# Kernel optimization log

Hardware: AMD Instinct MI355X
Metric: run time of the kernel (lower is better)

## Reference

```python
import jax, jax.numpy as jnp
import numpy as np
from jax import lax

B, S, H, I, E, TOP_K = 4, 4096, 2048, 1024, 8, 2


def setup_inputs() -> dict:
    key = jax.random.key(0)
    k1, k2, k3, k4, k5 = jax.random.split(key, 5)
    scale = 0.02  # realistic init scale so router logits are well-conditioned
    return {
        "x": jax.random.normal(k1, (B, S, H), dtype=jnp.float32),
        "gate_w": jax.random.normal(k2, (E, H), dtype=jnp.float32) * scale,
        "wg": jax.random.normal(k3, (E, H, I), dtype=jnp.float32) * scale,
        "wu": jax.random.normal(k4, (E, H, I), dtype=jnp.float32) * scale,
        "wd": jax.random.normal(k5, (E, I, H), dtype=jnp.float32) * scale,
    }


def reference(x, gate_w, wg, wu, wd):
    b, s, h = x.shape
    xt = x.reshape(b * s, h)                      # [T, H]
    router_logits = xt @ gate_w.T                 # [T, E]
    probs = jax.nn.softmax(router_logits, axis=-1)
    topk_w, topk_idx = lax.top_k(probs, TOP_K)    # [T, K]
    T = xt.shape[0]
    # combine[t, e] = routing weight of expert e for token t (0 if not in top-k)
    combine = jnp.zeros((T, E), xt.dtype).at[
        jnp.arange(T)[:, None], topk_idx
    ].set(topk_w)

    # scan over experts; each step is one grouped SwiGLU MLP over all tokens,
    # weighted by the (mostly-zero) combine column -> identical math to the
    # torch gather/index_add dispatch.
    def step(acc, ew):
        wgi, wui, wdi, c = ew                     # [H,I],[H,I],[I,H],[T]
        hdn = jax.nn.silu(xt @ wgi) * (xt @ wui)  # [T, I]
        return acc + c[:, None] * (hdn @ wdi), None

    acc, _ = lax.scan(step, jnp.zeros_like(xt), (wg, wu, wd, combine.T))
    return acc.reshape(b, s, h), router_logits
```

## Files before the change

### kernel.cpp

```cpp
#include <hip/hip_runtime.h>

#define T_TOK 16384
#define H_DIM 2048
#define I_DIM 1024
#define E_NUM 8

static const size_t F_WGT = 0;
static const size_t F_WUT = 33554432ull;
static const size_t F_XH  = 67108864ull;
static const size_t F_Y2  = 0;
static const size_t F_WDT = 134217728ull;
static const size_t F_HDN = 167772160ull;
static const size_t F_TOK = 234881024ull;
static const size_t F_WT  = 235405312ull;
static const size_t F_IDX = 235929600ull;
static const size_t F_CNT = 236060672ull;

typedef float f32x4 __attribute__((ext_vector_type(4)));
typedef _Float16 f16x8 __attribute__((ext_vector_type(8)));
typedef _Float16 f16x4 __attribute__((ext_vector_type(4)));

__device__ __forceinline__ void gload_lds16(const void* g, void* l) {
  __builtin_amdgcn_global_load_lds(
      (const __attribute__((address_space(1))) unsigned int*)g,
      (__attribute__((address_space(3))) unsigned int*)l, 16, 0, 0);
}

__global__ __launch_bounds__(256) void wconv_kernel(
    const float* __restrict__ wg, const float* __restrict__ wu,
    const float* __restrict__ wd, _Float16* __restrict__ wgT,
    _Float16* __restrict__ wuT, _Float16* __restrict__ wdT) {
  const int bx = blockIdx.x;
  const int w = bx >> 12;
  const int r2 = bx & 4095;
  const int e = r2 >> 9;
  const int t = r2 & 511;

  const float* src;
  _Float16* dst;
  int R, C;
  if (w == 0)      { src = wg; dst = wgT; R = H_DIM; C = I_DIM; }
  else if (w == 1) { src = wu; dst = wuT; R = H_DIM; C = I_DIM; }
  else             { src = wd; dst = wdT; R = I_DIM; C = H_DIM; }
  src += (size_t)e * R * C;
  dst += (size_t)e * R * C;

  const int tiles_c = C >> 6;
  const int tr = t / tiles_c;
  const int tc = t % tiles_c;

  __shared__ float tile[64][65];
  const int tid = threadIdx.x;

#pragma unroll
  for (int c = 0; c < 4; ++c) {
    const int q = c * 256 + tid;
    const int row = q >> 4;
    const int col4 = (q & 15) * 4;
    const float4 v = *(const float4*)(src + (size_t)(tr * 64 + row) * C + tc * 64 + col4);
    tile[row][col4 + 0] = v.x;
    tile[row][col4 + 1] = v.y;
    tile[row][col4 + 2] = v.z;
    tile[row][col4 + 3] = v.w;
  }
  __syncthreads();
#pragma unroll
  for (int c = 0; c < 4; ++c) {
    const int q = c * 256 + tid;
    const int row = q >> 4;
    const int col4 = (q & 15) * 4;
    f16x4 o = { (_Float16)tile[col4 + 0][row], (_Float16)tile[col4 + 1][row],
                (_Float16)tile[col4 + 2][row], (_Float16)tile[col4 + 3][row] };
    *(f16x4*)(dst + (size_t)(tc * 64 + row) * R + tr * 64 + col4) = o;
  }
}

__global__ __launch_bounds__(256) void router_kernel(
    const float* __restrict__ x, const float* __restrict__ gw,
    float* __restrict__ logits, int* __restrict__ tok_list,
    float* __restrict__ wt_list, int* __restrict__ idx2,
    int* __restrict__ counts, _Float16* __restrict__ xh) {
  const int lane = threadIdx.x & 63;
  const int wave = threadIdx.x >> 6;
  const int t = blockIdx.x * 4 + wave;
  const float* xr = x + (size_t)t * H_DIM;

  float xv[32];
#pragma unroll
  for (int j = 0; j < 32; ++j) xv[j] = xr[lane + j * 64];

  _Float16* xhr = xh + (size_t)t * H_DIM;
#pragma unroll
  for (int j = 0; j < 32; ++j) xhr[lane + j * 64] = (_Float16)xv[j];

  float lg[E_NUM];
#pragma unroll
  for (int e = 0; e < E_NUM; ++e) {
    const float* gr = gw + e * H_DIM;
    float s = 0.f;
#pragma unroll
    for (int j = 0; j < 32; ++j) s += xv[j] * gr[lane + j * 64];
#pragma unroll
    for (int off = 32; off > 0; off >>= 1) s += __shfl_xor(s, off, 64);
    lg[e] = s;
  }

  if (lane == 0) {
#pragma unroll
    for (int e = 0; e < E_NUM; ++e) logits[(size_t)t * E_NUM + e] = lg[e];
    float mx = lg[0];
#pragma unroll
    for (int e = 1; e < E_NUM; ++e) mx = fmaxf(mx, lg[e]);
    float se = 0.f;
#pragma unroll
    for (int e = 0; e < E_NUM; ++e) se += expf(lg[e] - mx);
    int i1 = 0; float b1 = lg[0];
#pragma unroll
    for (int e = 1; e < E_NUM; ++e) { if (lg[e] > b1) { b1 = lg[e]; i1 = e; } }
    int i2 = -1; float b2 = -1e30f;
#pragma unroll
    for (int e = 0; e < E_NUM; ++e) { if (e != i1 && lg[e] > b2) { b2 = lg[e]; i2 = e; } }
    const float p1 = expf(b1 - mx) / se;
    const float p2 = expf(b2 - mx) / se;
    int pos = atomicAdd(&counts[i1], 1);
    tok_list[i1 * T_TOK + pos] = t;
    wt_list[i1 * T_TOK + pos] = p1;
    idx2[t * 2] = (i1 << 16) | pos;
    pos = atomicAdd(&counts[i2], 1);
    tok_list[i2 * T_TOK + pos] = t;
    wt_list[i2 * T_TOK + pos] = p2;
    idx2[t * 2 + 1] = (i2 << 16) | pos;
  }
}

__global__ __launch_bounds__(256) void gemm1_kernel(
    const _Float16* __restrict__ xh, const _Float16* __restrict__ wgT,
    const _Float16* __restrict__ wuT, const int* __restrict__ tok_list,
    const int* __restrict__ counts, _Float16* __restrict__ hdn) {
  const int bx = blockIdx.x;
  const int cb = bx & 7;
  const int rb = (bx >> 3) & 127;
  const int e = bx >> 10;
  const int n_e = counts[e];
  const int row0 = rb * 128;
  if (row0 >= n_e) return;
  int goff = 0;
#pragma unroll
  for (int j = 0; j < E_NUM; ++j) goff += (j < e) ? counts[j] : 0;
  const int rem = min(128, n_e - row0);

  __shared__ int toks[128];
  __shared__ __attribute__((aligned(16))) _Float16 As[128 * 64];
  __shared__ __attribute__((aligned(16))) _Float16 Bg[128 * 64];
  __shared__ __attribute__((aligned(16))) _Float16 Bu[128 * 64];

  const int tid = threadIdx.x;
  if (tid < 128) {
    int idx = row0 + tid;
    if (idx > n_e - 1) idx = n_e - 1;
    toks[tid] = tok_list[e * T_TOK + idx];
  }
  __syncthreads();

  const int lane = tid & 63;
  const int wid = tid >> 6;
  const int wr = (wid >> 1) * 64;
  const int wcl = (wid & 1) * 64;
  const int n0 = cb * 128;

  const _Float16* wgTe = wgT + ((size_t)e * I_DIM + n0) * H_DIM;
  const _Float16* wuTe = wuT + ((size_t)e * I_DIM + n0) * H_DIM;

  const _Float16* aptr[4];
  int boff[4];
  int dofs[4];
#pragma unroll
  for (int c = 0; c < 4; ++c) {
    const int q = c * 256 + tid;
    const int rr = q >> 3;
    const int ch = q & 7;
    const int sch = ch ^ (rr & 7);
    aptr[c] = xh + (size_t)toks[rr] * H_DIM + sch * 8;
    boff[c] = rr * H_DIM + sch * 8;
    dofs[c] = q * 8;
  }

  const f32x4 z4 = {0.f, 0.f, 0.f, 0.f};
  f32x4 accg[4][4], accu[4][4];
#pragma unroll
  for (int m = 0; m < 4; ++m)
#pragma unroll
    for (int n = 0; n < 4; ++n) { accg[m][n] = z4; accu[m][n] = z4; }

  const int cl = lane & 15;
  const int kq = lane >> 4;

  for (int k0 = 0; k0 < H_DIM; k0 += 64) {
#pragma unroll
    for (int c = 0; c < 4; ++c) gload_lds16(aptr[c] + k0, As + dofs[c]);
#pragma unroll
    for (int c = 0; c < 4; ++c) gload_lds16(wgTe + boff[c] + k0, Bg + dofs[c]);
#pragma unroll
    for (int c = 0; c < 4; ++c) gload_lds16(wuTe + boff[c] + k0, Bu + dofs[c]);
    __syncthreads();

#pragma unroll
    for (int ks = 0; ks < 2; ++ks) {
      f16x8 af[4], bg[4], bu[4];
#pragma unroll
      for (int m = 0; m < 4; ++m) {
        const int row = wr + m * 16 + cl;
        af[m] = *(const f16x8*)(As + row * 64 + (((ks * 4 + kq) ^ (cl & 7)) * 8));
      }
#pragma unroll
      for (int n = 0; n < 4; ++n) {
        const int row = wcl + n * 16 + cl;
        const int off = row * 64 + (((ks * 4 + kq) ^ (cl & 7)) * 8);
        bg[n] = *(const f16x8*)(Bg + off);
        bu[n] = *(const f16x8*)(Bu + off);
      }
#pragma unroll
      for (int m = 0; m < 4; ++m)
#pragma unroll
        for (int n = 0; n < 4; ++n) {
          accg[m][n] = __builtin_amdgcn_mfma_f32_16x16x32_f16(af[m], bg[n], accg[m][n], 0, 0, 0);
          accu[m][n] = __builtin_amdgcn_mfma_f32_16x16x32_f16(af[m], bu[n], accu[m][n], 0, 0, 0);
        }
    }
    __syncthreads();
  }

  const int rq = lane >> 4;
#pragma unroll
  for (int m = 0; m < 4; ++m) {
#pragma unroll
    for (int r = 0; r < 4; ++r) {
      const int row = wr + m * 16 + rq * 4 + r;
      if (row < rem) {
        const size_t grow = (size_t)(goff + row0 + row);
#pragma unroll
        for (int n = 0; n < 4; ++n) {
          const float g = accg[m][n][r];
          const float u = accu[m][n][r];
          const float h = g / (1.f + __expf(-g)) * u;
          hdn[grow * I_DIM + n0 + wcl + n * 16 + cl] = (_Float16)h;
        }
      }
    }
  }
}

__global__ __launch_bounds__(256) void gemm2_kernel(
    const _Float16* __restrict__ hdn, const _Float16* __restrict__ wdT,
    const int* __restrict__ tok_list, const float* __restrict__ wt_list,
    const int* __restrict__ counts, _Float16* __restrict__ y2) {
  const int bx = blockIdx.x;
  const int nb = bx & 15;
  const int rb = (bx >> 4) & 127;
  const int e = bx >> 11;
  const int n_e = counts[e];
  const int row0 = rb * 128;
  if (row0 >= n_e) return;
  int goff = 0;
#pragma unroll
  for (int j = 0; j < E_NUM; ++j) goff += (j < e) ? counts[j] : 0;
  const int rem = min(128, n_e - row0);

  __shared__ float wts[128];
  __shared__ __attribute__((aligned(16))) _Float16 As[128 * 64];
  __shared__ __attribute__((aligned(16))) _Float16 Bs[128 * 64];

  const int tid = threadIdx.x;
  if (tid < 128) {
    int idx = row0 + tid;
    const bool valid = (idx < n_e);
    wts[tid] = valid ? wt_list[e * T_TOK + min(idx, n_e - 1)] : 0.f;
  }
  __syncthreads();

  const int lane = tid & 63;
  const int wid = tid >> 6;
  const int wr = (wid >> 1) * 64;
  const int wcl = (wid & 1) * 64;
  const int h0 = nb * 128;

  const _Float16* wdTe = wdT + ((size_t)e * H_DIM + h0) * I_DIM;
  const _Float16* hdnb = hdn + (size_t)(goff + row0) * I_DIM;

  const _Float16* aptr[4];
  int boff[4];
  int dofs[4];
#pragma unroll
  for (int c = 0; c < 4; ++c) {
    const int q = c * 256 + tid;
    const int rr = q >> 3;
    const int ch = q & 7;
    const int sch = ch ^ (rr & 7);
    const int rrc = min(rr, rem - 1);
    aptr[c] = hdnb + (size_t)rrc * I_DIM + sch * 8;
    boff[c] = rr * I_DIM + sch * 8;
    dofs[c] = q * 8;
  }

  const f32x4 z4 = {0.f, 0.f, 0.f, 0.f};
  f32x4 acc[4][4];
#pragma unroll
  for (int m = 0; m < 4; ++m)
#pragma unroll
    for (int n = 0; n < 4; ++n) acc[m][n] = z4;

  const int cl = lane & 15;
  const int kq = lane >> 4;

  for (int k0 = 0; k0 < I_DIM; k0 += 64) {
#pragma unroll
    for (int c = 0; c < 4; ++c) gload_lds16(aptr[c] + k0, As + dofs[c]);
#pragma unroll
    for (int c = 0; c < 4; ++c) gload_lds16(wdTe + boff[c] + k0, Bs + dofs[c]);
    __syncthreads();

#pragma unroll
    for (int ks = 0; ks < 2; ++ks) {
      f16x8 af[4], bf[4];
#pragma unroll
      for (int m = 0; m < 4; ++m) {
        const int row = wr + m * 16 + cl;
        af[m] = *(const f16x8*)(As + row * 64 + (((ks * 4 + kq) ^ (cl & 7)) * 8));
      }
#pragma unroll
      for (int n = 0; n < 4; ++n) {
        const int row = wcl + n * 16 + cl;
        bf[n] = *(const f16x8*)(Bs + row * 64 + (((ks * 4 + kq) ^ (cl & 7)) * 8));
      }
#pragma unroll
      for (int m = 0; m < 4; ++m)
#pragma unroll
        for (int n = 0; n < 4; ++n)
          acc[m][n] = __builtin_amdgcn_mfma_f32_16x16x32_f16(af[m], bf[n], acc[m][n], 0, 0, 0);
    }
    __syncthreads();
  }

  const int rq = lane >> 4;
#pragma unroll
  for (int m = 0; m < 4; ++m) {
#pragma unroll
    for (int r = 0; r < 4; ++r) {
      const int row = wr + m * 16 + rq * 4 + r;
      if (row < rem) {
        const float w = wts[row];
        _Float16* yrow = y2 + (size_t)(goff + row0 + row) * H_DIM + h0 + wcl;
#pragma unroll
        for (int n = 0; n < 4; ++n)
          yrow[n * 16 + cl] = (_Float16)(acc[m][n][r] * w);
      }
    }
  }
}

__global__ __launch_bounds__(256) void combine_kernel(
    const _Float16* __restrict__ y2, const int* __restrict__ idx2,
    const int* __restrict__ counts, float* __restrict__ out) {
  const int t = blockIdx.x;
  int pref[E_NUM];
  int run = 0;
#pragma unroll
  for (int e = 0; e < E_NUM; ++e) { pref[e] = run; run += counts[e]; }
  const int p0 = idx2[t * 2];
  const int p1 = idx2[t * 2 + 1];
  const size_t r0 = (size_t)(pref[p0 >> 16] + (p0 & 0xFFFF)) * H_DIM;
  const size_t r1 = (size_t)(pref[p1 >> 16] + (p1 & 0xFFFF)) * H_DIM;
  const int o = threadIdx.x * 8;
  const f16x8 a = *(const f16x8*)(y2 + r0 + o);
  const f16x8 b = *(const f16x8*)(y2 + r1 + o);
  float* orow = out + (size_t)t * H_DIM + o;
  float4 lo = { (float)a[0] + (float)b[0], (float)a[1] + (float)b[1],
                (float)a[2] + (float)b[2], (float)a[3] + (float)b[3] };
  float4 hi = { (float)a[4] + (float)b[4], (float)a[5] + (float)b[5],
                (float)a[6] + (float)b[6], (float)a[7] + (float)b[7] };
  *(float4*)orow = lo;
  *(float4*)(orow + 4) = hi;
}

extern "C" void kernel_launch(void* const* d_in, const int* in_sizes, int n_in,
                              void* d_out, int out_size, void* d_ws, size_t ws_size,
                              hipStream_t stream) {
  (void)in_sizes; (void)n_in; (void)out_size; (void)ws_size;
  const float* x      = (const float*)d_in[0];
  const float* gate_w = (const float*)d_in[1];
  const float* wg     = (const float*)d_in[2];
  const float* wu     = (const float*)d_in[3];
  const float* wd     = (const float*)d_in[4];
  float* out0 = (float*)d_out;
  float* out1 = out0 + (size_t)T_TOK * H_DIM;

  char* ws = (char*)d_ws;
  _Float16* wgT = (_Float16*)(ws + F_WGT);
  _Float16* wuT = (_Float16*)(ws + F_WUT);
  _Float16* xh  = (_Float16*)(ws + F_XH);
  _Float16* y2  = (_Float16*)(ws + F_Y2);
  _Float16* wdT = (_Float16*)(ws + F_WDT);
  _Float16* hdn = (_Float16*)(ws + F_HDN);
  int* tok_list = (int*)(ws + F_TOK);
  float* wt_list = (float*)(ws + F_WT);
  int* idx2 = (int*)(ws + F_IDX);
  int* counts = (int*)(ws + F_CNT);

  hipMemsetAsync(counts, 0, 64, stream);
  wconv_kernel<<<12288, 256, 0, stream>>>(wg, wu, wd, wgT, wuT, wdT);
  router_kernel<<<T_TOK / 4, 256, 0, stream>>>(x, gate_w, out1, tok_list, wt_list, idx2, counts, xh);
  gemm1_kernel<<<E_NUM * 128 * 8, 256, 0, stream>>>(xh, wgT, wuT, tok_list, counts, hdn);
  gemm2_kernel<<<E_NUM * 128 * 16, 256, 0, stream>>>(hdn, wdT, tok_list, wt_list, counts, y2);
  combine_kernel<<<T_TOK, 256, 0, stream>>>(y2, idx2, counts, out0);
}
```

Measured before the change: 1.630 ms.

## Double-buffer LDS tiles with K=32 steps to overlap loads with MFMA

```diff
diff --git a/kernel.cpp b/kernel.cpp
--- a/kernel.cpp
+++ b/kernel.cpp
@@ -150,9 +150,9 @@
   const int rem = min(128, n_e - row0);
 
   __shared__ int toks[128];
-  __shared__ __attribute__((aligned(16))) _Float16 As[128 * 64];
-  __shared__ __attribute__((aligned(16))) _Float16 Bg[128 * 64];
-  __shared__ __attribute__((aligned(16))) _Float16 Bu[128 * 64];
+  __shared__ __attribute__((aligned(16))) _Float16 As[2][128 * 32];
+  __shared__ __attribute__((aligned(16))) _Float16 Bg[2][128 * 32];
+  __shared__ __attribute__((aligned(16))) _Float16 Bu[2][128 * 32];
 
   const int tid = threadIdx.x;
   if (tid < 128) {
@@ -171,17 +171,16 @@
   const _Float16* wgTe = wgT + ((size_t)e * I_DIM + n0) * H_DIM;
   const _Float16* wuTe = wuT + ((size_t)e * I_DIM + n0) * H_DIM;
 
-  const _Float16* aptr[4];
-  int boff[4];
-  int dofs[4];
-#pragma unroll
-  for (int c = 0; c < 4; ++c) {
+  const _Float16* asrc[2];
+  int bofs[2], dofs[2];
+#pragma unroll
+  for (int c = 0; c < 2; ++c) {
     const int q = c * 256 + tid;
-    const int rr = q >> 3;
-    const int ch = q & 7;
-    const int sch = ch ^ (rr & 7);
-    aptr[c] = xh + (size_t)toks[rr] * H_DIM + sch * 8;
-    boff[c] = rr * H_DIM + sch * 8;
+    const int rr = q >> 2;
+    const int ch = q & 3;
+    const int sch = ch ^ ((rr >> 1) & 3);
+    asrc[c] = xh + (size_t)toks[rr] * H_DIM + sch * 8;
+    bofs[c] = rr * H_DIM + sch * 8;
     dofs[c] = q * 8;
   }
 
@@ -195,39 +194,61 @@
   const int cl = lane & 15;
   const int kq = lane >> 4;
 
-  for (int k0 = 0; k0 < H_DIM; k0 += 64) {
-#pragma unroll
-    for (int c = 0; c < 4; ++c) gload_lds16(aptr[c] + k0, As + dofs[c]);
-#pragma unroll
-    for (int c = 0; c < 4; ++c) gload_lds16(wgTe + boff[c] + k0, Bg + dofs[c]);
-#pragma unroll
-    for (int c = 0; c < 4; ++c) gload_lds16(wuTe + boff[c] + k0, Bu + dofs[c]);
-    __syncthreads();
-
-#pragma unroll
-    for (int ks = 0; ks < 2; ++ks) {
-      f16x8 af[4], bg[4], bu[4];
-#pragma unroll
-      for (int m = 0; m < 4; ++m) {
-        const int row = wr + m * 16 + cl;
-        af[m] = *(const f16x8*)(As + row * 64 + (((ks * 4 + kq) ^ (cl & 7)) * 8));
+  int aoff[4], boffr[4];
+#pragma unroll
+  for (int m = 0; m < 4; ++m) {
+    const int row = wr + m * 16 + cl;
+    aoff[m] = row * 32 + ((kq ^ ((row >> 1) & 3)) * 8);
+  }
+#pragma unroll
+  for (int n = 0; n < 4; ++n) {
+    const int row = wcl + n * 16 + cl;
+    boffr[n] = row * 32 + ((kq ^ ((row >> 1) & 3)) * 8);
+  }
+
+#pragma unroll
+  for (int c = 0; c < 2; ++c) {
+    gload_lds16(asrc[c], &As[0][0] + dofs[c]);
+    gload_lds16(wgTe + bofs[c], &Bg[0][0] + dofs[c]);
+    gload_lds16(wuTe + bofs[c], &Bu[0][0] + dofs[c]);
+  }
+  asm volatile("s_waitcnt vmcnt(0)" ::: "memory");
+  __builtin_amdgcn_s_barrier();
+  __builtin_amdgcn_sched_barrier(0);
+
+  const int NK = H_DIM / 32;
+  for (int t = 0; t < NK; ++t) {
+    const int cur = t & 1;
+    if (t + 1 < NK) {
+      const int kn = (t + 1) * 32;
+#pragma unroll
+      for (int c = 0; c < 2; ++c) {
+        gload_lds16(asrc[c] + kn, &As[cur ^ 1][0] + dofs[c]);
+        gload_lds16(wgTe + bofs[c] + kn, &Bg[cur ^ 1][0] + dofs[c]);
+        gload_lds16(wuTe + bofs[c] + kn, &Bu[cur ^ 1][0] + dofs[c]);
       }
+    }
+    const _Float16* Ac = &As[cur][0];
+    const _Float16* Gc = &Bg[cur][0];
+    const _Float16* Uc = &Bu[cur][0];
+    f16x8 af[4], bg[4], bu[4];
+#pragma unroll
+    for (int m = 0; m < 4; ++m) af[m] = *(const f16x8*)(Ac + aoff[m]);
+#pragma unroll
+    for (int n = 0; n < 4; ++n) {
+      bg[n] = *(const f16x8*)(Gc + boffr[n]);
+      bu[n] = *(const f16x8*)(Uc + boffr[n]);
+    }
+#pragma unroll
+    for (int m = 0; m < 4; ++m)
 #pragma unroll
       for (int n = 0; n < 4; ++n) {
-        const int row = wcl + n * 16 + cl;
-        const int off = row * 64 + (((ks * 4 + kq) ^ (cl & 7)) * 8);
-        bg[n] = *(const f16x8*)(Bg + off);
-        bu[n] = *(const f16x8*)(Bu + off);
+        accg[m][n] = __builtin_amdgcn_mfma_f32_16x16x32_f16(af[m], bg[n], accg[m][n], 0, 0, 0);
+        accu[m][n] = __builtin_amdgcn_mfma_f32_16x16x32_f16(af[m], bu[n], accu[m][n], 0, 0, 0);
       }
-#pragma unroll
-      for (int m = 0; m < 4; ++m)
-#pragma unroll
-        for (int n = 0; n < 4; ++n) {
-          accg[m][n] = __builtin_amdgcn_mfma_f32_16x16x32_f16(af[m], bg[n], accg[m][n], 0, 0, 0);
-          accu[m][n] = __builtin_amdgcn_mfma_f32_16x16x32_f16(af[m], bu[n], accu[m][n], 0, 0, 0);
-        }
-    }
-    __syncthreads();
+    asm volatile("s_waitcnt vmcnt(0)" ::: "memory");
+    __builtin_amdgcn_s_barrier();
+    __builtin_amdgcn_sched_barrier(0);
   }
 
   const int rq = lane >> 4;
@@ -267,8 +288,8 @@
   const int rem = min(128, n_e - row0);
 
   __shared__ float wts[128];
-  __shared__ __attribute__((aligned(16))) _Float16 As[128 * 64];
-  __shared__ __attribute__((aligned(16))) _Float16 Bs[128 * 64];
+  __shared__ __attribute__((aligned(16))) _Float16 As[2][128 * 32];
+  __shared__ __attribute__((aligned(16))) _Float16 Bs[2][128 * 32];
 
   const int tid = threadIdx.x;
   if (tid < 128) {
@@ -287,18 +308,17 @@
   const _Float16* wdTe = wdT + ((size_t)e * H_DIM + h0) * I_DIM;
   const _Float16* hdnb = hdn + (size_t)(goff + row0) * I_DIM;
 
-  const _Float16* aptr[4];
-  int boff[4];
-  int dofs[4];
-#pragma unroll
-  for (int c = 0; c < 4; ++c) {
+  const _Float16* asrc[2];
+  int bofs[2], dofs[2];
+#pragma unroll
+  for (int c = 0; c < 2; ++c) {
     const int q = c * 256 + tid;
-    const int rr = q >> 3;
-    const int ch = q & 7;
-    const int sch = ch ^ (rr & 7);
+    const int rr = q >> 2;
+    const int ch = q & 3;
+    const int sch = ch ^ ((rr >> 1) & 3);
     const int rrc = min(rr, rem - 1);
-    aptr[c] = hdnb + (size_t)rrc * I_DIM + sch * 8;
-    boff[c] = rr * I_DIM + sch * 8;
+    asrc[c] = hdnb + (size_t)rrc * I_DIM + sch * 8;
+    bofs[c] = rr * I_DIM + sch * 8;
     dofs[c] = q * 8;
   }
 
@@ -312,33 +332,53 @@
   const int cl = lane & 15;
   const int kq = lane >> 4;
 
-  for (int k0 = 0; k0 < I_DIM; k0 += 64) {
-#pragma unroll
-    for (int c = 0; c < 4; ++c) gload_lds16(aptr[c] + k0, As + dofs[c]);
-#pragma unroll
-    for (int c = 0; c < 4; ++c) gload_lds16(wdTe + boff[c] + k0, Bs + dofs[c]);
-    __syncthreads();
-
-#pragma unroll
-    for (int ks = 0; ks < 2; ++ks) {
-      f16x8 af[4], bf[4];
-#pragma unroll
-      for (int m = 0; m < 4; ++m) {
-        const int row = wr + m * 16 + cl;
-        af[m] = *(const f16x8*)(As + row * 64 + (((ks * 4 + kq) ^ (cl & 7)) * 8));
+  int aoff[4], boffr[4];
+#pragma unroll
+  for (int m = 0; m < 4; ++m) {
+    const int row = wr + m * 16 + cl;
+    aoff[m] = row * 32 + ((kq ^ ((row >> 1) & 3)) * 8);
+  }
+#pragma unroll
+  for (int n = 0; n < 4; ++n) {
+    const int row = wcl + n * 16 + cl;
+    boffr[n] = row * 32 + ((kq ^ ((row >> 1) & 3)) * 8);
+  }
+
+#pragma unroll
+  for (int c = 0; c < 2; ++c) {
+    gload_lds16(asrc[c], &As[0][0] + dofs[c]);
+    gload_lds16(wdTe + bofs[c], &Bs[0][0] + dofs[c]);
+  }
+  asm volatile("s_waitcnt vmcnt(0)" ::: "memory");
+  __builtin_amdgcn_s_barrier();
+  __builtin_amdgcn_sched_barrier(0);
+
+  const int NK = I_DIM / 32;
+  for (int t = 0; t < NK; ++t) {
+    const int cur = t & 1;
+    if (t + 1 < NK) {
+      const int kn = (t + 1) * 32;
+#pragma unroll
+      for (int c = 0; c < 2; ++c) {
+        gload_lds16(asrc[c] + kn, &As[cur ^ 1][0] + dofs[c]);
+        gload_lds16(wdTe + bofs[c] + kn, &Bs[cur ^ 1][0] + dofs[c]);
       }
-#pragma unroll
-      for (int n = 0; n < 4; ++n) {
-        const int row = wcl + n * 16 + cl;
-        bf[n] = *(const f16x8*)(Bs + row * 64 + (((ks * 4 + kq) ^ (cl & 7)) * 8));
-      }
-#pragma unroll
-      for (int m = 0; m < 4; ++m)
-#pragma unroll
-        for (int n = 0; n < 4; ++n)
-          acc[m][n] = __builtin_amdgcn_mfma_f32_16x16x32_f16(af[m], bf[n], acc[m][n], 0, 0, 0);
     }
-    __syncthreads();
+    const _Float16* Ac = &As[cur][0];
+    const _Float16* Bc = &Bs[cur][0];
+    f16x8 af[4], bf[4];
+#pragma unroll
+    for (int m = 0; m < 4; ++m) af[m] = *(const f16x8*)(Ac + aoff[m]);
+#pragma unroll
+    for (int n = 0; n < 4; ++n) bf[n] = *(const f16x8*)(Bc + boffr[n]);
+#pragma unroll
+    for (int m = 0; m < 4; ++m)
+#pragma unroll
+      for (int n = 0; n < 4; ++n)
+        acc[m][n] = __builtin_amdgcn_mfma_f32_16x16x32_f16(af[m], bf[n], acc[m][n], 0, 0, 0);
+    asm volatile("s_waitcnt vmcnt(0)" ::: "memory");
+    __builtin_amdgcn_s_barrier();
+    __builtin_amdgcn_sched_barrier(0);
   }
 
   const int rq = lane >> 4;
```

Measured after the change: 1.450 ms. 11.1% less time.
